# Optimization experiments

Hardware: AMD Instinct MI355X
Metric: run time of the kernel (lower is better)

## Reference

```python
import jax, jax.numpy as jnp
import numpy as np

IMG = 64            # image_height = image_width = 64
NPTS = 300          # n_pts_per_ray
MIN_DEPTH, MAX_DEPTH = 0.1, 3.0
GRID = 16           # latent_dim -> 16^3 voxel grid
VOXEL_SIZE = 0.1
FOV_DEG = 60.0      # pytorch3d FoVPerspectiveCameras default
B = 8               # number of cameras / latents
EPS = 1e-10         # EmissionAbsorptionRaymarcher eps


def _look_at(eye, at):
    # pytorch3d look_at_view_transform: row-vector convention x_view = x_world @ R + T
    up = np.array([0.0, 1.0, 0.0])
    z = at - eye; z = z / np.linalg.norm(z)
    x = np.cross(up, z); x = x / np.linalg.norm(x)
    y = np.cross(z, x); y = y / np.linalg.norm(y)
    R = np.stack([x, y, z], axis=1)  # columns are camera axes
    T = -eye @ R
    return R, T


def setup_inputs():
    rng = np.random.default_rng(0)
    Rs, Ts = [], []
    for _ in range(B):
        eye = rng.standard_normal(3) * np.array([0.01, 0.0001, 0.01])
        at = rng.standard_normal(3) * 0.01
        R, T = _look_at(eye, at)
        Rs.append(R); Ts.append(T)

    def lin(fan_in, fan_out):
        bound = 1.0 / np.sqrt(fan_in)  # torch Linear default init
        W = rng.uniform(-bound, bound, size=(fan_in, fan_out))
        b = rng.uniform(-bound, bound, size=(fan_out,))
        return jnp.asarray(W, jnp.float32), jnp.asarray(b, jnp.float32)

    W1, b1 = lin(30, 60)
    W2, b2 = lin(60, 480)
    W3, b3 = lin(480, 4 * GRID ** 3)
    zs = jnp.asarray(rng.standard_normal((B, 30)), jnp.float32)
    return {"zs": zs, "W1": W1, "b1": b1, "W2": W2, "b2": b2, "W3": W3, "b3": b3,
            "R": jnp.asarray(np.stack(Rs), jnp.float32),
            "T": jnp.asarray(np.stack(Ts), jnp.float32)}


def _grid_sample3d(vol, xyz):
    # vol: (C, D, H, W); xyz: (..., 3) in [-1, 1]; trilinear, align_corners=True, zero padding
    C, D, H, W = vol.shape
    batch_shape = xyz.shape[:-1]
    p = xyz.reshape(-1, 3)
    ix = (p[:, 0] + 1.0) * 0.5 * (W - 1)
    iy = (p[:, 1] + 1.0) * 0.5 * (H - 1)
    iz = (p[:, 2] + 1.0) * 0.5 * (D - 1)
    x0 = jnp.floor(ix); y0 = jnp.floor(iy); z0 = jnp.floor(iz)
    tx = ix - x0; ty = iy - y0; tz = iz - z0
    out = jnp.zeros((C, p.shape[0]), vol.dtype)
    for dx, wx in ((0, 1.0 - tx), (1, tx)):
        for dy, wy in ((0, 1.0 - ty), (1, ty)):
            for dz, wz in ((0, 1.0 - tz), (1, tz)):
                xf, yf, zf = x0 + dx, y0 + dy, z0 + dz
                valid = ((xf >= 0) & (xf <= W - 1) & (yf >= 0) & (yf <= H - 1)
                         & (zf >= 0) & (zf <= D - 1))
                xi = jnp.clip(xf, 0, W - 1).astype(jnp.int32)
                yi = jnp.clip(yf, 0, H - 1).astype(jnp.int32)
                zi = jnp.clip(zf, 0, D - 1).astype(jnp.int32)
                w = jnp.where(valid, wx * wy * wz, 0.0)
                out = out + w[None, :] * vol[:, zi, yi, xi]
    return jnp.moveaxis(out.reshape((C,) + batch_shape), 0, -1)


def _forward(zs, W1, b1, W2, b2, W3, b3, R, T):
    # latent MLP -> (B, 4, 16, 16, 16) volume (1 density channel + 3 color channels)
    h = jax.nn.sigmoid(zs @ W1 + b1)
    h = jax.nn.sigmoid(h @ W2 + b2)
    lat = jax.nn.sigmoid(h @ W3 + b3).reshape(-1, 4, GRID, GRID, GRID)
    densities = lat[:, 0:1]   # (B,1,D,H,W)
    colors = lat[:, 1:4]      # (B,3,D,H,W)

    # NDCGridRaysampler pixel-center grid (pytorch3d NDC: +x left, +y up, row 0 at max y)
    half_pix = 1.0 / IMG
    xs = jnp.linspace(1.0 - half_pix, -1.0 + half_pix, IMG)
    ys = jnp.linspace(1.0 - half_pix, -1.0 + half_pix, IMG)
    f = 1.0 / jnp.tan(jnp.deg2rad(FOV_DEG) / 2.0)  # focal from fov, aspect=1
    dir_cam = jnp.stack([jnp.broadcast_to(xs[None, :] / f, (IMG, IMG)),
                         jnp.broadcast_to(ys[:, None] / f, (IMG, IMG)),
                         jnp.ones((IMG, IMG))], axis=-1)  # (H,W,3)
    Rt = jnp.swapaxes(R, 1, 2)                             # view->world rotation
    dirs_w = jnp.einsum('hwc,bcd->bhwd', dir_cam, Rt)      # (B,H,W,3)
    origins_w = jnp.einsum('bc,bcd->bd', -T, Rt)           # camera centers (B,3)

    depths = jnp.linspace(MIN_DEPTH, MAX_DEPTH, NPTS)
    pts = origins_w[:, None, None, None, :] + dirs_w[:, :, :, None, :] * depths[None, None, None, :, None]
    half_extent = (GRID - 1) * VOXEL_SIZE * 0.5            # pytorch3d Volumes world->local scale
    local = pts / half_extent                              # (B,H,W,P,3)

    sigma = jax.vmap(_grid_sample3d)(densities, local)[..., 0]  # (B,H,W,P)
    feats = jax.vmap(_grid_sample3d)(colors, local)             # (B,H,W,P,3)

    # EmissionAbsorptionRaymarcher (surface_thickness=1)
    a = (1.0 + EPS) - sigma
    cp = jnp.cumprod(a, axis=-1)
    absorption = jnp.concatenate([jnp.ones_like(cp[..., :1]), cp[..., :-1]], axis=-1)
    weights = sigma * absorption
    rgb = jnp.sum(weights[..., None] * feats, axis=-2)          # (B,H,W,3)
    opacity = 1.0 - jnp.prod(1.0 - sigma, axis=-1, keepdims=True)
    return jnp.concatenate([rgb, opacity], axis=-1)             # (B,H,W,4)


def reference(zs, W1, b1, W2, b2, W3, b3, R, T):
    imgs = _forward(zs, W1, b1, W2, b2, W3, b3, R, T)
    return imgs[..., 3:4], imgs[..., 0:3]
```

## Files before the change

kernel.cpp:

```cpp
#include <hip/hip_runtime.h>
#include <hip/hip_bf16.h>

#define IMG 64
#define NPTS 300
#define GRIDN 16
#define BATCH 8
#define KSLICES 32
#define KROWS 15

typedef __hip_bfloat16 bf16;

__device__ __forceinline__ float sigm(float x) { return 1.0f / (1.0f + __expf(-x)); }
__device__ __forceinline__ float lo_bf(unsigned u) { return __uint_as_float(u << 16); }
__device__ __forceinline__ float hi_bf(unsigned u) { return __uint_as_float(u & 0xffff0000u); }
__device__ __forceinline__ float us_bf(unsigned short u) {
    return __uint_as_float(((unsigned)u) << 16);
}

template <typename T>
__device__ __forceinline__ float ldv(const void* p, int i);
template <>
__device__ __forceinline__ float ldv<float>(const void* p, int i) { return ((const float*)p)[i]; }
template <>
__device__ __forceinline__ float ldv<bf16>(const void* p, int i) {
    return __bfloat162float(((const bf16*)p)[i]);
}

__device__ __forceinline__ void sniff(const void* W1, int* sflag, int t) {
    if (t < 64) {
        float m = 0.0f;
        for (int i = t; i < 1800; i += 64) {
            float v = fabsf(__bfloat162float(((const bf16*)W1)[i]));
            if (!(v < 1e30f)) v = 1e30f;
            m = fmaxf(m, v);
        }
#pragma unroll
        for (int d = 1; d < 64; d <<= 1) m = fmaxf(m, __shfl_xor(m, d));
        if (t == 0) *sflag = (m > 4.0f) ? 1 : 0;
    }
}

template <typename T>
__device__ void prep_body(const void* zs, const void* b1, const void* W1, const void* W2,
                          const void* b2, const void* W3, float* __restrict__ partial) {
    __shared__ float z[BATCH][30];
    __shared__ float h1[BATCH][60];
    __shared__ float h2s[BATCH][KROWS];
    int t = threadIdx.x;
    int jb = blockIdx.x;
    int s = blockIdx.y;
    int i0 = s * KROWS;

    if (t < 240) {
        int b = t / 30, i = t - b * 30;
        z[b][i] = ldv<T>(zs, t);
    }
    __syncthreads();
    if (t < 480) {
        int b = t / 60, j = t - b * 60;
        float acc = ldv<T>(b1, j);
#pragma unroll
        for (int i = 0; i < 30; ++i) acc = fmaf(z[b][i], ldv<T>(W1, i * 60 + j), acc);
        h1[b][j] = sigm(acc);
    }
    __syncthreads();
    if (t < BATCH * KROWS) {
        int b = t / KROWS, rr = t - b * KROWS;
        int col = i0 + rr;
        float acc = ldv<T>(b2, col);
#pragma unroll
        for (int i = 0; i < 60; ++i) acc = fmaf(h1[b][i], ldv<T>(W2, i * 480 + col), acc);
        h2s[b][rr] = sigm(acc);
    }
    __syncthreads();

    int th = t & 255;
    int bh = t >> 8;
    int j0 = jb * 1024 + th * 4;
    float acc[4][4];
#pragma unroll
    for (int b = 0; b < 4; ++b)
#pragma unroll
        for (int c = 0; c < 4; ++c) acc[b][c] = 0.0f;

#pragma unroll
    for (int i = 0; i < KROWS; ++i) {
        float w0, w1, w2, w3v;
        if (sizeof(T) == 2) {
            ushort4 q = *(const ushort4*)((const unsigned short*)W3 + (size_t)(i0 + i) * 16384 + j0);
            w0 = us_bf(q.x); w1 = us_bf(q.y); w2 = us_bf(q.z); w3v = us_bf(q.w);
        } else {
            float4 q = *(const float4*)((const float*)W3 + (size_t)(i0 + i) * 16384 + j0);
            w0 = q.x; w1 = q.y; w2 = q.z; w3v = q.w;
        }
#pragma unroll
        for (int b = 0; b < 4; ++b) {
            float h = h2s[bh * 4 + b][i];
            acc[b][0] = fmaf(h, w0, acc[b][0]);
            acc[b][1] = fmaf(h, w1, acc[b][1]);
            acc[b][2] = fmaf(h, w2, acc[b][2]);
            acc[b][3] = fmaf(h, w3v, acc[b][3]);
        }
    }
#pragma unroll
    for (int b = 0; b < 4; ++b) {
        float4 st = {acc[b][0], acc[b][1], acc[b][2], acc[b][3]};
        *(float4*)(partial + ((size_t)(s * BATCH + bh * 4 + b) << 14) + j0) = st;
    }
}

__global__ __launch_bounds__(512) void prep_kernel(const void* zs, const void* W1,
                                                   const void* b1, const void* W2,
                                                   const void* b2, const void* W3,
                                                   float* __restrict__ partial,
                                                   int* __restrict__ flag) {
    __shared__ int sflag;
    int t = threadIdx.x;
    sniff(W1, &sflag, t);
    __syncthreads();
    if (blockIdx.x == 0 && blockIdx.y == 0 && t == 0) *flag = sflag;
    if (sflag)
        prep_body<float>(zs, b1, W1, W2, b2, W3, partial);
    else
        prep_body<bf16>(zs, b1, W1, W2, b2, W3, partial);
}

__global__ __launch_bounds__(256) void w3_reduce_kernel(const float* __restrict__ partial,
                                                        const void* b3, bf16* __restrict__ volbf,
                                                        const int* __restrict__ flag) {
    int tid = blockIdx.x * 256 + threadIdx.x;
    int b = tid >> 14, j = tid & 16383;
    float a = 0.0f;
#pragma unroll
    for (int s = 0; s < KSLICES; ++s) a += partial[((size_t)(s * BATCH + b) << 14) + j];
    a += (*flag) ? ldv<float>(b3, j) : ldv<bf16>(b3, j);
    a = sigm(a);
    int c = j >> 12, v = j & 4095;
    volbf[(size_t)((b << 12) + v) * 4 + c] = __float2bfloat16(a);
}

__global__ __launch_bounds__(256) void render_kernel(const void* Rm, const void* Tm,
                                                     const bf16* __restrict__ volbf, void* out,
                                                     const int* __restrict__ flag) {
    __shared__ uint2 vox[8000];
    int t = threadIdx.x;
    int rayBase = blockIdx.x * 64;
    int b = rayBase >> 12;
    const uint2* src = (const uint2*)(volbf + (size_t)b * 4096 * 4);
    for (int i = t; i < 8000; i += 256) vox[i] = make_uint2(0u, 0u);
    __syncthreads();
    for (int i = t; i < 4096; i += 256) {
        int x = i & 15, y = (i >> 4) & 15, zc = i >> 8;
        vox[(zc + 2) * 400 + (y + 2) * 20 + (x + 2)] = src[i];
    }
    __syncthreads();

    int f32out = *flag;
    int ray = rayBase + (t >> 2);
    int seg = t & 3;
    int pix = ray & 4095;
    int h = pix >> 6, w = pix & 63;

    const float inv_f = 0.57735026919f;
    float dcx = (0.984375f - 0.03125f * (float)w) * inv_f;
    float dcy = (0.984375f - 0.03125f * (float)h) * inv_f;

    float R[9], Tv[3];
    if (f32out) {
#pragma unroll
        for (int i = 0; i < 9; ++i) R[i] = ((const float*)Rm)[b * 9 + i];
#pragma unroll
        for (int i = 0; i < 3; ++i) Tv[i] = ((const float*)Tm)[b * 3 + i];
    } else {
#pragma unroll
        for (int i = 0; i < 9; ++i) R[i] = __bfloat162float(((const bf16*)Rm)[b * 9 + i]);
#pragma unroll
        for (int i = 0; i < 3; ++i) Tv[i] = __bfloat162float(((const bf16*)Tm)[b * 3 + i]);
    }

    float dx_ = dcx * R[0] + dcy * R[1] + R[2];
    float dy_ = dcx * R[3] + dcy * R[4] + R[5];
    float dz_ = dcx * R[6] + dcy * R[7] + R[8];
    float ox = -(Tv[0] * R[0] + Tv[1] * R[1] + Tv[2] * R[2]);
    float oy = -(Tv[0] * R[3] + Tv[1] * R[4] + Tv[2] * R[5]);
    float oz = -(Tv[0] * R[6] + Tv[1] * R[7] + Tv[2] * R[8]);

    float tA = -1e30f, tB = 1e30f;
    bool miss = false;
    {
        float dd[3] = {dx_, dy_, dz_}, oo[3] = {ox, oy, oz};
#pragma unroll
        for (int a = 0; a < 3; ++a) {
            if (fabsf(dd[a]) > 1e-8f) {
                float inv = 1.0f / dd[a];
                float ra = (-0.85f - oo[a]) * inv, rb = (0.85f - oo[a]) * inv;
                tA = fmaxf(tA, fminf(ra, rb));
                tB = fminf(tB, fmaxf(ra, rb));
            } else if (fabsf(oo[a]) >= 0.85f) {
                miss = true;
            }
        }
    }
    const float step = 2.9f / 299.0f;
    const float inv_step = 299.0f / 2.9f;
    int ilo = 0, ihi = -1;
    if (!miss && tB > tA) {
        float flo = fmaxf(-2.0f, fminf(302.0f, ceilf((tA - 0.1f) * inv_step)));
        float fhi = fmaxf(-2.0f, fminf(302.0f, floorf((tB - 0.1f) * inv_step)));
        ilo = (int)flo - 1;
        ihi = (int)fhi + 1;
        if (ilo < 0) ilo = 0;
        if (ihi > 299) ihi = 299;
    }
    int n = ihi - ilo + 1;
    if (n < 0) n = 0;
    int s0 = ilo + (n * seg) / 4;
    int s1 = ilo + (n * (seg + 1)) / 4;

    float cr = 0.f, cg = 0.f, cb = 0.f, Pa = 1.f;
    for (int i = s0; i < s1; ++i) {
        float tt = 0.1f + step * (float)i;
        float ix = fmaf(fmaf(tt, dx_, ox), 10.0f, 7.5f);
        float iy = fmaf(fmaf(tt, dy_, oy), 10.0f, 7.5f);
        float iz = fmaf(fmaf(tt, dz_, oz), 10.0f, 7.5f);
        float fx = floorf(ix), fy = floorf(iy), fz = floorf(iz);
        float txf = ix - fx, tyf = iy - fy, tzf = iz - fz;
        int x0 = (int)fx, y0 = (int)fy, z0 = (int)fz;

        int base = z0 * 400 + y0 * 20 + x0 + 842;
        float wx0 = 1.0f - txf, wy0 = 1.0f - tyf, wz0 = 1.0f - tzf;
        float wxy00 = wx0 * wy0, wxy10 = txf * wy0, wxy01 = wx0 * tyf, wxy11 = txf * tyf;

        float sx = 0.f, sr = 0.f, sg = 0.f, sb = 0.f;
#define CORNP(W, OFF)                          \
    {                                          \
        uint2 q = vox[base + (OFF)];           \
        float wgt_ = (W);                      \
        sx = fmaf(wgt_, lo_bf(q.x), sx);       \
        sr = fmaf(wgt_, hi_bf(q.x), sr);       \
        sg = fmaf(wgt_, lo_bf(q.y), sg);       \
        sb = fmaf(wgt_, hi_bf(q.y), sb);       \
    }
        CORNP(wxy00 * wz0, 0)
        CORNP(wxy10 * wz0, 1)
        CORNP(wxy01 * wz0, 20)
        CORNP(wxy11 * wz0, 21)
        CORNP(wxy00 * tzf, 400)
        CORNP(wxy10 * tzf, 401)
        CORNP(wxy01 * tzf, 420)
        CORNP(wxy11 * tzf, 421)
#undef CORNP

        float wgt = sx * Pa;
        cr = fmaf(wgt, sr, cr);
        cg = fmaf(wgt, sg, cg);
        cb = fmaf(wgt, sb, cb);
        Pa *= (1.0f - sx);
    }

#pragma unroll
    for (int d = 1; d < 4; d <<= 1) {
        float o_cr = __shfl_xor(cr, d);
        float o_cg = __shfl_xor(cg, d);
        float o_cb = __shfl_xor(cb, d);
        float o_Pa = __shfl_xor(Pa, d);
        bool first = ((seg & d) == 0);
        cr = first ? fmaf(Pa, o_cr, cr) : fmaf(o_Pa, cr, o_cr);
        cg = first ? fmaf(Pa, o_cg, cg) : fmaf(o_Pa, cg, o_cg);
        cb = first ? fmaf(Pa, o_cb, cb) : fmaf(o_Pa, cb, o_cb);
        Pa *= o_Pa;
    }

    if (seg == 0) {
        if (f32out) {
            float* of = (float*)out;
            of[ray] = 1.0f - Pa;
            float* orgb = of + BATCH * IMG * IMG;
            orgb[ray * 3 + 0] = cr;
            orgb[ray * 3 + 1] = cg;
            orgb[ray * 3 + 2] = cb;
        } else {
            bf16* ob = (bf16*)out;
            ob[ray] = __float2bfloat16(1.0f - Pa);
            bf16* orgb = ob + BATCH * IMG * IMG;
            orgb[ray * 3 + 0] = __float2bfloat16(cr);
            orgb[ray * 3 + 1] = __float2bfloat16(cg);
            orgb[ray * 3 + 2] = __float2bfloat16(cb);
        }
    }
}

extern "C" void kernel_launch(void* const* d_in, const int* in_sizes, int n_in,
                              void* d_out, int out_size, void* d_ws, size_t ws_size,
                              hipStream_t stream) {
    const void* zs = d_in[0];
    const void* W1 = d_in[1];
    const void* b1 = d_in[2];
    const void* W2 = d_in[3];
    const void* b2 = d_in[4];
    const void* W3 = d_in[5];
    const void* b3 = d_in[6];
    const void* Rm = d_in[7];
    const void* Tm = d_in[8];

    bf16* volbf = (bf16*)d_ws;
    float* partial = (float*)((char*)d_ws + 262144);
    int* flag = (int*)((char*)d_ws + 262144 + (size_t)KSLICES * BATCH * 16384 * 4);

    hipLaunchKernelGGL(prep_kernel, dim3(16, KSLICES), dim3(512), 0, stream, zs, W1, b1, W2,
                       b2, W3, partial, flag);
    hipLaunchKernelGGL(w3_reduce_kernel, dim3(512), dim3(256), 0, stream, partial, b3, volbf,
                       flag);
    hipLaunchKernelGGL(render_kernel, dim3(512), dim3(256), 0, stream, Rm, Tm, volbf, d_out,
                       flag);
}
```

Measured before the change: 124.7 us.

## Stage W3 slabs through LDS with larger K-slices in prep kernel

Doubles the K-rows each prep block handles (halving the K-slice count and the partial-sum traffic) and loads the W3 slab cooperatively into a 60 KB shared buffer with 16-byte loads before computing. The loads are issued before a barrier so they overlap the layer-2 work, and the fp32 path takes two passes. This cuts partial writes and the reduce kernel's reads, but the large LDS use lowers occupancy and leaves half as many blocks.

New measurement: 133.9 us. 1.07x slower.

```diff
diff --git a/kernel.cpp b/kernel.cpp
--- a/kernel.cpp
+++ b/kernel.cpp
@@ -5,8 +5,8 @@
 #define NPTS 300
 #define GRIDN 16
 #define BATCH 8
-#define KSLICES 32
-#define KROWS 15
+#define KSLICES 16
+#define KROWS 30
 
 typedef __hip_bfloat16 bf16;
 
@@ -40,12 +40,17 @@
     }
 }
 
+struct PrepSmem {
+    alignas(16) unsigned char w3t[61440];
+    float z[BATCH][30];
+    float h1[BATCH][60];
+    float h2s[BATCH][KROWS];
+};
+
 template <typename T>
 __device__ void prep_body(const void* zs, const void* b1, const void* W1, const void* W2,
-                          const void* b2, const void* W3, float* __restrict__ partial) {
-    __shared__ float z[BATCH][30];
-    __shared__ float h1[BATCH][60];
-    __shared__ float h2s[BATCH][KROWS];
+                          const void* b2, const void* W3, float* __restrict__ partial,
+                          PrepSmem* sm) {
     int t = threadIdx.x;
     int jb = blockIdx.x;
     int s = blockIdx.y;
@@ -53,59 +58,96 @@
 
     if (t < 240) {
         int b = t / 30, i = t - b * 30;
-        z[b][i] = ldv<T>(zs, t);
+        sm->z[b][i] = ldv<T>(zs, t);
     }
     __syncthreads();
     if (t < 480) {
         int b = t / 60, j = t - b * 60;
         float acc = ldv<T>(b1, j);
 #pragma unroll
-        for (int i = 0; i < 30; ++i) acc = fmaf(z[b][i], ldv<T>(W1, i * 60 + j), acc);
-        h1[b][j] = sigm(acc);
-    }
-    __syncthreads();
-    if (t < BATCH * KROWS) {
-        int b = t / KROWS, rr = t - b * KROWS;
+        for (int i = 0; i < 30; ++i) acc = fmaf(sm->z[b][i], ldv<T>(W1, i * 60 + j), acc);
+        sm->h1[b][j] = sigm(acc);
+    }
+    __syncthreads();
+    if (t < 240) {
+        int b = t / 30, rr = t - b * 30;
         int col = i0 + rr;
         float acc = ldv<T>(b2, col);
 #pragma unroll
-        for (int i = 0; i < 60; ++i) acc = fmaf(h1[b][i], ldv<T>(W2, i * 480 + col), acc);
-        h2s[b][rr] = sigm(acc);
-    }
-    __syncthreads();
+        for (int i = 0; i < 60; ++i) acc = fmaf(sm->h1[b][i], ldv<T>(W2, i * 480 + col), acc);
+        sm->h2s[b][rr] = sigm(acc);
+    }
 
     int th = t & 255;
     int bh = t >> 8;
+    float acc[4][4];
+#pragma unroll
+    for (int b = 0; b < 4; ++b)
+#pragma unroll
+        for (int c = 0; c < 4; ++c) acc[b][c] = 0.0f;
+
+    const int PASSES = (sizeof(T) == 2) ? 1 : 2;
+    const int RPP = (sizeof(T) == 2) ? 30 : 15;
+
+    for (int p = 0; p < PASSES; ++p) {
+        uint4 st[8];
+#pragma unroll
+        for (int i = 0; i < 8; ++i) {
+            int v = t + 512 * i;
+            if (v < 3840) {
+                int byte = v << 4;
+                int row, off;
+                if (sizeof(T) == 2) { row = byte >> 11; off = byte & 2047; }
+                else { row = byte >> 12; off = byte & 4095; }
+                const char* src = (const char*)W3 +
+                                  (size_t)(i0 + p * RPP + row) * (16384 * sizeof(T)) +
+                                  (size_t)jb * (1024 * sizeof(T)) + (size_t)off;
+                st[i] = *(const uint4*)src;
+            }
+        }
+        __syncthreads();
+#pragma unroll
+        for (int i = 0; i < 8; ++i) {
+            int v = t + 512 * i;
+            if (v < 3840) *(uint4*)&sm->w3t[v << 4] = st[i];
+        }
+        __syncthreads();
+
+        if (sizeof(T) == 2) {
+#pragma unroll 6
+            for (int r = 0; r < 30; ++r) {
+                ushort4 q = *(const ushort4*)&sm->w3t[r * 2048 + th * 8];
+                float w0 = us_bf(q.x), w1 = us_bf(q.y), w2 = us_bf(q.z), w3v = us_bf(q.w);
+#pragma unroll
+                for (int b = 0; b < 4; ++b) {
+                    float h = sm->h2s[bh * 4 + b][r];
+                    acc[b][0] = fmaf(h, w0, acc[b][0]);
+                    acc[b][1] = fmaf(h, w1, acc[b][1]);
+                    acc[b][2] = fmaf(h, w2, acc[b][2]);
+                    acc[b][3] = fmaf(h, w3v, acc[b][3]);
+                }
+            }
+        } else {
+#pragma unroll 5
+            for (int r = 0; r < 15; ++r) {
+                float4 q = *(const float4*)&sm->w3t[r * 4096 + th * 16];
+#pragma unroll
+                for (int b = 0; b < 4; ++b) {
+                    float h = sm->h2s[bh * 4 + b][p * 15 + r];
+                    acc[b][0] = fmaf(h, q.x, acc[b][0]);
+                    acc[b][1] = fmaf(h, q.y, acc[b][1]);
+                    acc[b][2] = fmaf(h, q.z, acc[b][2]);
+                    acc[b][3] = fmaf(h, q.w, acc[b][3]);
+                }
+            }
+        }
+    }
+
     int j0 = jb * 1024 + th * 4;
-    float acc[4][4];
-#pragma unroll
-    for (int b = 0; b < 4; ++b)
-#pragma unroll
-        for (int c = 0; c < 4; ++c) acc[b][c] = 0.0f;
-
-#pragma unroll
-    for (int i = 0; i < KROWS; ++i) {
-        float w0, w1, w2, w3v;
-        if (sizeof(T) == 2) {
-            ushort4 q = *(const ushort4*)((const unsigned short*)W3 + (size_t)(i0 + i) * 16384 + j0);
-            w0 = us_bf(q.x); w1 = us_bf(q.y); w2 = us_bf(q.z); w3v = us_bf(q.w);
-        } else {
-            float4 q = *(const float4*)((const float*)W3 + (size_t)(i0 + i) * 16384 + j0);
-            w0 = q.x; w1 = q.y; w2 = q.z; w3v = q.w;
-        }
-#pragma unroll
-        for (int b = 0; b < 4; ++b) {
-            float h = h2s[bh * 4 + b][i];
-            acc[b][0] = fmaf(h, w0, acc[b][0]);
-            acc[b][1] = fmaf(h, w1, acc[b][1]);
-            acc[b][2] = fmaf(h, w2, acc[b][2]);
-            acc[b][3] = fmaf(h, w3v, acc[b][3]);
-        }
-    }
 #pragma unroll
     for (int b = 0; b < 4; ++b) {
-        float4 st = {acc[b][0], acc[b][1], acc[b][2], acc[b][3]};
-        *(float4*)(partial + ((size_t)(s * BATCH + bh * 4 + b) << 14) + j0) = st;
+        float4 stv = {acc[b][0], acc[b][1], acc[b][2], acc[b][3]};
+        *(float4*)(partial + ((size_t)(s * BATCH + bh * 4 + b) << 14) + j0) = stv;
     }
 }
 
@@ -114,15 +156,16 @@
                                                    const void* b2, const void* W3,
                                                    float* __restrict__ partial,
                                                    int* __restrict__ flag) {
+    __shared__ PrepSmem sm;
     __shared__ int sflag;
     int t = threadIdx.x;
     sniff(W1, &sflag, t);
     __syncthreads();
     if (blockIdx.x == 0 && blockIdx.y == 0 && t == 0) *flag = sflag;
     if (sflag)
-        prep_body<float>(zs, b1, W1, W2, b2, W3, partial);
+        prep_body<float>(zs, b1, W1, W2, b2, W3, partial, &sm);
     else
-        prep_body<bf16>(zs, b1, W1, W2, b2, W3, partial);
+        prep_body<bf16>(zs, b1, W1, W2, b2, W3, partial, &sm);
 }
 
 __global__ __launch_bounds__(256) void w3_reduce_kernel(const float* __restrict__ partial,
```
